# Performance work log

Hardware: AMD Instinct MI355X
Metric: run time of the kernel (lower is better)

The kernel has to match this reference:

```python
import jax, jax.numpy as jnp
import numpy as np

HID, NH, HD = 1024, 16, 64
WIN = 512
DFF, NE, TOPK = 4096, 8, 2
B, S = 1, 2048
EPS = 1e-6


def _rope_rotation_matrix(seq_len, head_dim):
    # Block-diagonal 2x2 rotation matrices per position (standard RoPE as a fused matrix).
    pos = np.arange(seq_len, dtype=np.float64)
    inv_freq = 1.0 / (10000.0 ** (np.arange(0, head_dim, 2, dtype=np.float64) / head_dim))
    ang = pos[:, None] * inv_freq[None, :]            # [S, HD/2]
    c, s = np.cos(ang), np.sin(ang)
    R = np.zeros((seq_len, head_dim, head_dim), np.float32)
    i = np.arange(0, head_dim, 2)
    R[:, i, i] = c
    R[:, i + 1, i + 1] = c
    R[:, i, i + 1] = -s
    R[:, i + 1, i] = s
    return jnp.asarray(R)


def setup_inputs() -> dict:
    key = jax.random.key(0)
    ks = jax.random.split(key, 10)
    init = lambda k, shape, scale=0.02: (jax.random.normal(k, shape, jnp.float32) * scale)
    return {
        "x": jax.random.normal(ks[0], (B, S, HID), jnp.float32),
        "rotation_matrix": _rope_rotation_matrix(S, HD),
        "rms1_w": jnp.ones((HID,), jnp.float32),
        "wq": init(ks[1], (HID, HID)),
        "wk": init(ks[2], (HID, HID)),
        "wv": init(ks[3], (HID, HID)),
        "wo": init(ks[4], (HID, HID)),
        "rms2_w": jnp.ones((HID,), jnp.float32),
        "gate_w": init(ks[5], (HID, NE)),
        "w1": init(ks[6], (NE, HID, DFF)),
        "w2": init(ks[7], (NE, DFF, HID)),
        "w3": init(ks[8], (NE, HID, DFF)),
    }


def _rmsnorm(x, w):
    return x * jax.lax.rsqrt(jnp.mean(x * x, axis=-1, keepdims=True) + EPS) * w


def reference(x, rotation_matrix, rms1_w, wq, wk, wv, wo, rms2_w, gate_w, w1, w2, w3):
    b, s, _ = x.shape
    # --- sliding-window attention with fused RoPE rotation matrix ---
    y = _rmsnorm(x, rms1_w)
    q = (y @ wq).reshape(b, s, NH, HD).transpose(0, 2, 1, 3)  # bhsd
    k = (y @ wk).reshape(b, s, NH, HD).transpose(0, 2, 1, 3)
    v = (y @ wv).reshape(b, s, NH, HD).transpose(0, 2, 1, 3)
    q = jnp.einsum('bhsd,sde->bhse', q, rotation_matrix)
    k = jnp.einsum('bhsd,sde->bhse', k, rotation_matrix)
    scores = jnp.einsum('bhqd,bhkd->bhqk', q, k) / np.float32(np.sqrt(HD))
    idx = jnp.arange(s)
    mask = (idx[:, None] >= idx[None, :]) & (idx[:, None] - idx[None, :] < WIN)
    scores = jnp.where(mask[None, None], scores, jnp.float32(-1e9))
    att = jax.nn.softmax(scores, axis=-1)
    attn_out = jnp.einsum('bhqk,bhkd->bhqd', att, v)
    attn_out = attn_out.transpose(0, 2, 1, 3).reshape(b, s, HID) @ wo
    x = x + attn_out
    # --- MoE SwiGLU FFN with top-k routing ---
    y = _rmsnorm(x, rms2_w)
    t = y.reshape(b * s, HID)                                  # [T, D]
    logits = t @ gate_w                                        # [T, E]
    top_v, top_i = jax.lax.top_k(logits, TOPK)
    gates = jax.nn.softmax(top_v, axis=-1)                     # [T, K]
    w_full = jnp.zeros((b * s, NE), t.dtype).at[
        jnp.arange(b * s)[:, None], top_i].set(gates)          # [T, E] sparse routing weights
    h = jax.nn.silu(jnp.einsum('td,edf->etf', t, w1)) * jnp.einsum('td,edf->etf', t, w3)
    expert_out = jnp.einsum('etf,efd->etd', h, w2)             # [E, T, D]
    moe = jnp.einsum('te,etd->td', w_full, expert_out).reshape(b, s, HID)
    return x + moe
```

## Files before the change

kernel.cpp:

```cpp
#include <hip/hip_runtime.h>
#include <hip/hip_bf16.h>
#include <stdint.h>


#define S_ 2048
#define HID_ 1024
#define NH_ 16
#define HD_ 64
#define WIN_ 512
#define DFF_ 4096
#define NE_ 8

typedef unsigned short u16;
typedef __attribute__((ext_vector_type(8))) short short8;
typedef __attribute__((ext_vector_type(4))) float f32x4;

__device__ __forceinline__ u16 f2bf(float f) {
  union { float f; unsigned u; } v; v.f = f;
  unsigned r = (v.u + 0x7FFFu + ((v.u >> 16) & 1u)) >> 16;
  return (u16)r;
}
__device__ __forceinline__ float bf2f(u16 b) {
  union { unsigned u; float f; } v; v.u = ((unsigned)b) << 16;
  return v.f;
}

__device__ __forceinline__ void gload16(const void* g, void* l) {
  __builtin_amdgcn_global_load_lds(
      (const __attribute__((address_space(1))) void*)g,
      (__attribute__((address_space(3))) void*)l, 16, 0, 0);
}

template <int N>
__device__ __forceinline__ void waitcnt_vm() {
  static_assert(N == 0 || N == 2 || N == 4 || N == 6 || N == 8 || N == 12 ||
                N == 16 || N == 24, "unsupported vmcnt");
  if constexpr (N == 0) asm volatile("s_waitcnt vmcnt(0)" ::: "memory");
  else if constexpr (N == 2) asm volatile("s_waitcnt vmcnt(2)" ::: "memory");
  else if constexpr (N == 4) asm volatile("s_waitcnt vmcnt(4)" ::: "memory");
  else if constexpr (N == 6) asm volatile("s_waitcnt vmcnt(6)" ::: "memory");
  else if constexpr (N == 8) asm volatile("s_waitcnt vmcnt(8)" ::: "memory");
  else if constexpr (N == 12) asm volatile("s_waitcnt vmcnt(12)" ::: "memory");
  else if constexpr (N == 16) asm volatile("s_waitcnt vmcnt(16)" ::: "memory");
  else if constexpr (N == 24) asm volatile("s_waitcnt vmcnt(24)" ::: "memory");
}

__global__ __launch_bounds__(512) void convT_f32_k(const float* __restrict__ Wa,
                                                   const float* __restrict__ Wb,
                                                   int zsplit,
                                                   u16* __restrict__ WT,
                                                   int K, int N, size_t matStride) {
  __shared__ alignas(16) char T[256 * 264];
  int z = blockIdx.z;
  const float* Wm = (z < zsplit ? Wa + (size_t)z * matStride
                                : Wb + (size_t)(z - zsplit) * matStride);
  u16* WTm = WT + (size_t)z * matStride;
  int n0 = blockIdx.x * 128, k0 = blockIdx.y * 256;
  int tid = threadIdx.x;
  int mq = tid & 31, tr_ = tid >> 5;
#pragma unroll
  for (int p = 0; p < 16; ++p) {
    int k = p * 16 + tr_;
    float4 v = *(const float4*)&Wm[(size_t)(k0 + k) * N + n0 + mq * 4];
    uint2 pk;
    pk.x = (unsigned)f2bf(v.x) | ((unsigned)f2bf(v.y) << 16);
    pk.y = (unsigned)f2bf(v.z) | ((unsigned)f2bf(v.w) << 16);
    *(uint2*)(T + k * 264 + ((mq ^ ((k >> 2) & 31)) << 3)) = pk;
  }
  __syncthreads();
#pragma unroll
  for (int p = 0; p < 8; ++p) {
    int n = p * 16 + tr_;
    int un = n >> 2, lo2 = (n & 3) * 2;
    short8 o;
#pragma unroll
    for (int j = 0; j < 8; ++j) {
      int k = mq * 8 + j;
      ((u16*)&o)[j] =
          *(const u16*)(T + k * 264 + ((un ^ ((k >> 2) & 31)) << 3) + lo2);
    }
    *(short8*)&WTm[(size_t)(n0 + n) * K + k0 + mq * 8] = o;
  }
}

__global__ __launch_bounds__(512) void convT_qkvo_k(const float* __restrict__ wq,
                                                    const float* __restrict__ wk,
                                                    const float* __restrict__ wv,
                                                    const float* __restrict__ wo,
                                                    u16* __restrict__ outT) {
  __shared__ alignas(16) char T[256 * 264];
  int z = blockIdx.z;
  const float* Wm = (z == 0) ? wq : (z == 1) ? wk : (z == 2) ? wv : wo;
  u16* WTm = outT + (size_t)z * HID_ * HID_;
  int n0 = blockIdx.x * 128, k0 = blockIdx.y * 256;
  int tid = threadIdx.x;
  int mq = tid & 31, tr_ = tid >> 5;
#pragma unroll
  for (int p = 0; p < 16; ++p) {
    int k = p * 16 + tr_;
    float4 v = *(const float4*)&Wm[(size_t)(k0 + k) * HID_ + n0 + mq * 4];
    uint2 pk;
    pk.x = (unsigned)f2bf(v.x) | ((unsigned)f2bf(v.y) << 16);
    pk.y = (unsigned)f2bf(v.z) | ((unsigned)f2bf(v.w) << 16);
    *(uint2*)(T + k * 264 + ((mq ^ ((k >> 2) & 31)) << 3)) = pk;
  }
  __syncthreads();
#pragma unroll
  for (int p = 0; p < 8; ++p) {
    int n = p * 16 + tr_;
    int un = n >> 2, lo2 = (n & 3) * 2;
    short8 o;
#pragma unroll
    for (int j = 0; j < 8; ++j) {
      int k = mq * 8 + j;
      ((u16*)&o)[j] =
          *(const u16*)(T + k * 264 + ((un ^ ((k >> 2) & 31)) << 3) + lo2);
    }
    *(short8*)&WTm[(size_t)(n0 + n) * HID_ + k0 + mq * 8] = o;
  }
}

__global__ __launch_bounds__(256) void convT_u16_k(const u16* __restrict__ W,
                                                   u16* __restrict__ WT,
                                                   int K, int N, size_t matStride) {
  __shared__ u16 t[64][66];
  const u16* Wm = W + (size_t)blockIdx.z * matStride;
  u16* WTm = WT + (size_t)blockIdx.z * matStride;
  int n0 = blockIdx.x * 64, k0 = blockIdx.y * 64;
  int tid = threadIdx.x;
  int c2 = (tid & 31) * 2, rr = tid >> 5;
#pragma unroll
  for (int it = 0; it < 8; ++it) {
    int r = it * 8 + rr;
    unsigned vv = *(const unsigned*)&Wm[(size_t)(k0 + r) * N + n0 + c2];
    t[c2][r] = (u16)vv;
    t[c2 + 1][r] = (u16)(vv >> 16);
  }
  __syncthreads();
#pragma unroll
  for (int it = 0; it < 8; ++it) {
    int n = it * 8 + rr;
    unsigned pk = (unsigned)t[n][c2] | ((unsigned)t[n][c2 + 1] << 16);
    *(unsigned*)&WTm[(size_t)(n0 + n) * K + k0 + c2] = pk;
  }
}

__global__ __launch_bounds__(256) void rope_tab_k(const float* __restrict__ rot,
                                                  float* __restrict__ cost,
                                                  float* __restrict__ sint) {
  int id = blockIdx.x * 256 + threadIdx.x;
  if (id >= S_ * 32) return;
  int s = id >> 5, j = id & 31;
  cost[id] = rot[(size_t)s * 4096 + (size_t)(2 * j) * 64 + 2 * j];
  sint[id] = rot[(size_t)s * 4096 + (size_t)(2 * j + 1) * 64 + 2 * j];
}

__global__ __launch_bounds__(256) void rms1_k(const float* __restrict__ x,
                                              const float* __restrict__ rw,
                                              u16* __restrict__ y) {
  int row = blockIdx.x, tid = threadIdx.x;
  const float4 v = *(const float4*)&x[(size_t)row * HID_ + tid * 4];
  float ss = v.x * v.x + v.y * v.y + v.z * v.z + v.w * v.w;
#pragma unroll
  for (int o = 32; o; o >>= 1) ss += __shfl_xor(ss, o);
  __shared__ float red[4];
  if ((tid & 63) == 0) red[tid >> 6] = ss;
  __syncthreads();
  float rstd = rsqrtf((red[0] + red[1] + red[2] + red[3]) * (1.f / HID_) + 1e-6f);
  const float4 w4 = *(const float4*)&rw[tid * 4];
  ushort4 o4;
  o4.x = f2bf(v.x * rstd * w4.x);
  o4.y = f2bf(v.y * rstd * w4.y);
  o4.z = f2bf(v.z * rstd * w4.z);
  o4.w = f2bf(v.w * rstd * w4.w);
  *(ushort4*)&y[(size_t)row * HID_ + tid * 4] = o4;
}

__global__ __launch_bounds__(256) void rms2_gate_k(const float* __restrict__ x2,
                                                   const float* __restrict__ rw,
                                                   const float* __restrict__ gw,
                                                   u16* __restrict__ y2,
                                                   float* __restrict__ logits) {
  int row = blockIdx.x, tid = threadIdx.x;
  int wv = tid >> 6, ln = tid & 63;
  const float4 v = *(const float4*)&x2[(size_t)row * HID_ + tid * 4];
  float ss = v.x * v.x + v.y * v.y + v.z * v.z + v.w * v.w;
#pragma unroll
  for (int o = 32; o; o >>= 1) ss += __shfl_xor(ss, o);
  __shared__ float red[4];
  __shared__ float lred[4][8];
  if (ln == 0) red[wv] = ss;
  __syncthreads();
  float rstd = rsqrtf((red[0] + red[1] + red[2] + red[3]) * (1.f / HID_) + 1e-6f);
  const float4 w4 = *(const float4*)&rw[tid * 4];
  float yv[4];
  yv[0] = v.x * rstd * w4.x; yv[1] = v.y * rstd * w4.y;
  yv[2] = v.z * rstd * w4.z; yv[3] = v.w * rstd * w4.w;
  ushort4 o4;
  o4.x = f2bf(yv[0]); o4.y = f2bf(yv[1]); o4.z = f2bf(yv[2]); o4.w = f2bf(yv[3]);
  *(ushort4*)&y2[(size_t)row * HID_ + tid * 4] = o4;
  float le[8] = {0, 0, 0, 0, 0, 0, 0, 0};
  int d0 = tid * 4;
#pragma unroll
  for (int j = 0; j < 4; ++j) {
    const float* grow = &gw[(size_t)(d0 + j) * NE_];
#pragma unroll
    for (int e = 0; e < 8; ++e) le[e] += yv[j] * grow[e];
  }
#pragma unroll
  for (int e = 0; e < 8; ++e) {
    float t = le[e];
#pragma unroll
    for (int o = 32; o; o >>= 1) t += __shfl_xor(t, o);
    le[e] = t;
  }
  if (ln == 0)
#pragma unroll
    for (int e = 0; e < 8; ++e) lred[wv][e] = le[e];
  __syncthreads();
  if (tid < 8)
    logits[(size_t)row * NE_ + tid] =
        lred[0][tid] + lred[1][tid] + lred[2][tid] + lred[3][tid];
}

__global__ __launch_bounds__(1024) void route_k(const float* __restrict__ logits,
                                                int* __restrict__ topi,
                                                float* __restrict__ topg,
                                                int* __restrict__ counts,
                                                int* __restrict__ ebase,
                                                int* __restrict__ slot_token,
                                                int* __restrict__ slot_of) {
  __shared__ int cnt[8], bas[8], rnk[8];
  int tid = threadIdx.x;
  if (tid < 8) { cnt[tid] = 0; rnk[tid] = 0; }
  __syncthreads();
  int e0[2], e1[2];
  float g0[2], g1[2];
#pragma unroll
  for (int s = 0; s < 2; ++s) {
    int t = tid * 2 + s;
    const float* lg = &logits[(size_t)t * NE_];
    float v0 = -1e30f; int i0 = 0;
#pragma unroll
    for (int e = 0; e < 8; ++e) {
      float x = lg[e];
      if (x > v0) { v0 = x; i0 = e; }
    }
    float v1 = -1e30f; int i1 = 0;
#pragma unroll
    for (int e = 0; e < 8; ++e) {
      if (e == i0) continue;
      float x = lg[e];
      if (x > v1) { v1 = x; i1 = e; }
    }
    float ex = __expf(v1 - v0);
    e0[s] = i0; e1[s] = i1;
    g0[s] = 1.f / (1.f + ex);
    g1[s] = ex / (1.f + ex);
    topi[t * 2] = i0; topi[t * 2 + 1] = i1;
    topg[t * 2] = g0[s]; topg[t * 2 + 1] = g1[s];
    atomicAdd(&cnt[i0], 1);
    atomicAdd(&cnt[i1], 1);
  }
  __syncthreads();
  if (tid == 0) {
    int s = 0;
    for (int e = 0; e < 8; ++e) { bas[e] = s; s += cnt[e]; }
  }
  __syncthreads();
#pragma unroll
  for (int s = 0; s < 2; ++s) {
    int t = tid * 2 + s;
    int p0 = bas[e0[s]] + atomicAdd(&rnk[e0[s]], 1);
    int p1 = bas[e1[s]] + atomicAdd(&rnk[e1[s]], 1);
    slot_token[p0] = t; slot_token[p1] = t;
    slot_of[t * 2] = p0; slot_of[t * 2 + 1] = p1;
  }
  if (tid < 8) { counts[tid] = cnt[tid]; ebase[tid] = bas[tid]; }
}

template <int MODE, int SLOTS>
__global__ __launch_bounds__(256, (SLOTS <= 3 ? 3 : (SLOTS <= 5 ? 2 : 1)))
void gemm3_k(
    const u16* __restrict__ A, const u16* __restrict__ B0,
    const u16* __restrict__ B1, const u16* __restrict__ B2, int K,
    const int* __restrict__ ecnt, const int* __restrict__ ebase,
    const float* __restrict__ cost, const float* __restrict__ sint,
    const float* __restrict__ xres, float* __restrict__ outf,
    u16* __restrict__ o0, u16* __restrict__ o1, u16* __restrict__ o2) {
  constexpr int WVM = 4 * (SLOTS - 2);
  __shared__ alignas(16) char smem[SLOTS * 16384];

  int n0 = blockIdx.x * 128, m0 = blockIdx.y * 128;
  int cnt = 0, base = 0, kc = 0;
  const u16* Bp;
  u16* outb = o0;
  float* pout = outf;
  int rope = 0;
  if constexpr (MODE == 0) {
    int z = blockIdx.z;
    Bp = (z == 0) ? B0 : (z == 1) ? B1 : B2;
    outb = (z == 0) ? o0 : (z == 1) ? o1 : o2;
    rope = (z < 2) ? 1 : 0;
  } else if constexpr (MODE == 1) {
    Bp = B0;
  } else if constexpr (MODE == 4) {
    int e = blockIdx.z >> 1;
    kc = blockIdx.z & 1;
    cnt = ecnt[e]; base = ebase[e];
    if (m0 >= cnt) return;
    Bp = B0 + (size_t)e * HID_ * DFF_;
    pout = outf + (size_t)kc * ((size_t)2 * S_ * HID_);
  } else {
    int e = blockIdx.z;
    cnt = ecnt[e]; base = ebase[e];
    if (m0 >= cnt) return;
    Bp = B0 + (size_t)e * HID_ * DFF_;
  }

  int tid = threadIdx.x, w = tid >> 6, l = tid & 63, lo = l & 15, g = l >> 4;
  int wm = w >> 1, wn = w & 1;
  int KT = K >> 5;
  size_t rb = (MODE == 4) ? (size_t)DFF_ * 2 : (size_t)K * 2;
  size_t kcoff = (MODE == 4) ? (size_t)kc * (size_t)(DFF_ / 2) * 2 : 0;

  int lrow = l >> 2, lu = l & 3;
  const char* pA[2];
  const char* pB[2];
  int ldOff[2];
#pragma unroll
  for (int j = 0; j < 2; ++j) {
    int rA = j * 64 + w * 16 + lrow;
    int swz = (lu ^ ((rA >> 1) & 3)) << 4;
    size_t arow;
    if constexpr (MODE == 3 || MODE == 4) {
      arow = (size_t)(base + min(m0 + rA, cnt - 1));
    } else {
      arow = (size_t)(m0 + rA);
    }
    pA[j] = (const char*)A + arow * rb + kcoff + swz;
    pB[j] = (const char*)Bp + (size_t)(n0 + rA) * rb + kcoff + swz;
    ldOff[j] = (j * 64 + w * 16) * 64;
  }

  auto stage = [&](int t) {
    char* s = smem + (t % SLOTS) * 16384;
    size_t kb = (size_t)t * 64;
    gload16(pA[0] + kb, s + ldOff[0]);
    gload16(pA[1] + kb, s + ldOff[1]);
    gload16(pB[0] + kb, s + 8192 + ldOff[0]);
    gload16(pB[1] + kb, s + 8192 + ldOff[1]);
  };

  f32x4 acc[4][4];
#pragma unroll
  for (int i = 0; i < 4; ++i)
#pragma unroll
    for (int j = 0; j < 4; ++j) acc[i][j] = (f32x4){0.f, 0.f, 0.f, 0.f};

#pragma unroll
  for (int s = 0; s < SLOTS - 1; ++s) stage(min(s, KT - 1));
  waitcnt_vm<WVM>();
  __builtin_amdgcn_s_barrier();

  for (int t = 0; t < KT; ++t) {
    char* s = smem + (t % SLOTS) * 16384;
    stage(min(t + SLOTS - 1, KT - 1));
    short8 afr[4], bfr[4];
#pragma unroll
    for (int mi = 0; mi < 4; ++mi) {
      int r = wm * 64 + mi * 16 + lo;
      afr[mi] = *(const short8*)(s + r * 64 + ((g ^ ((r >> 1) & 3)) << 4));
    }
#pragma unroll
    for (int ni = 0; ni < 4; ++ni) {
      int r = wn * 64 + ni * 16 + lo;
      bfr[ni] = *(const short8*)(s + 8192 + r * 64 + ((g ^ ((r >> 1) & 3)) << 4));
    }
    asm volatile("s_waitcnt lgkmcnt(0)" ::: "memory");
    __builtin_amdgcn_s_setprio(1);
#pragma unroll
    for (int mi = 0; mi < 4; ++mi)
#pragma unroll
      for (int ni = 0; ni < 4; ++ni)
        acc[mi][ni] = __builtin_amdgcn_mfma_f32_16x16x32_bf16(afr[mi], bfr[ni], acc[mi][ni], 0, 0, 0);
    __builtin_amdgcn_s_setprio(0);
    if (t + 1 < KT)
      waitcnt_vm<WVM>();
    else
      waitcnt_vm<0>();
    __builtin_amdgcn_s_barrier();
  }
  asm volatile("s_waitcnt vmcnt(0) lgkmcnt(0)" ::: "memory");

#pragma unroll
  for (int mi = 0; mi < 4; ++mi) {
    int lr = wm * 64 + mi * 16 + g * 4;
#pragma unroll
    for (int ni = 0; ni < 4; ++ni) {
      int c = n0 + wn * 64 + ni * 16 + lo;
#pragma unroll
      for (int r = 0; r < 4; ++r) {
        float v = acc[mi][ni][r];
        if constexpr (MODE == 0) {
          int row = m0 + lr + r;
          float p = __shfl_xor(v, 1);
          if (rope) {
            int dd = c & 63;
            float co = cost[(size_t)row * 32 + (dd >> 1)];
            float si = sint[(size_t)row * 32 + (dd >> 1)];
            v = (dd & 1) ? (co * v - si * p) : (co * v + si * p);
          }
          outb[((size_t)(c >> 6) * S_ + row) * HD_ + (c & 63)] = f2bf(v);
        } else if constexpr (MODE == 1) {
          int row = m0 + lr + r;
          outf[(size_t)row * HID_ + c] = v + xres[(size_t)row * HID_ + c];
        } else if constexpr (MODE == 4) {
          int m = m0 + lr + r;
          if (m < cnt) pout[(size_t)(base + m) * HID_ + c] = v;
        } else {
          int m = m0 + lr + r;
          if (m < cnt) outb[(size_t)(base + m) * HID_ + c] = f2bf(v);
        }
      }
    }
  }
}

__global__ __launch_bounds__(512, 2) void gemm5_k(
    const u16* __restrict__ A, const u16* __restrict__ B0,
    const u16* __restrict__ B1, int K, const int* __restrict__ ecnt,
    const int* __restrict__ ebase, const int* __restrict__ slot_token,
    u16* __restrict__ o0, u16* __restrict__ o1) {
  constexpr int BM = 256;
  constexpr int MROW = 128;
  constexpr int MI = 8;
  constexpr int MH = 4;
  constexpr int ABYTES = BM * 128;
  __shared__ alignas(16) char smem[ABYTES * 4];
  char* ldsA = smem;
  char* ldsB = smem + 2 * ABYTES;

  int n0 = blockIdx.x * BM, m0 = blockIdx.y * BM;
  int e = blockIdx.z >> 1, mat = blockIdx.z & 1;
  int cnt = ecnt[e], base = ebase[e];
  if (m0 >= cnt) return;
  const u16* Bp = (mat ? B1 : B0) + (size_t)e * DFF_ * HID_;
  u16* outb = mat ? o1 : o0;

  int tid = threadIdx.x, w = tid >> 6, l = tid & 63, lo = l & 15, g = l >> 4;
  int wm = w >> 2, wn = w & 3;
  int KT = K >> 6;
  size_t rb = (size_t)K * 2;

  int lrow = l >> 3, lu = l & 7;
  const char* pA[4];
  const char* pB[4];
  int ldOff[4];
#pragma unroll
  for (int j = 0; j < 4; ++j) {
    int rA = j * 64 + w * 8 + lrow;
    int swz = (lu ^ (rA & 7)) << 4;
    size_t arow = (size_t)slot_token[base + min(m0 + rA, cnt - 1)];
    pA[j] = (const char*)A + arow * rb + swz;
    pB[j] = (const char*)Bp + (size_t)(n0 + rA) * rb + swz;
    ldOff[j] = (j * 64 + w * 8) * 128;
  }

  auto stA = [&](int t, int j) {
    gload16(pA[j] + (size_t)t * 128, ldsA + (t & 1) * ABYTES + ldOff[j]);
  };
  auto stB = [&](int t, int j) {
    gload16(pB[j] + (size_t)t * 128, ldsB + (t & 1) * ABYTES + ldOff[j]);
  };
  auto rdA = [&](int d, int mi, int kh) {
    int row = wm * MROW + mi * 16 + lo;
    return *(const short8*)(ldsA + d * ABYTES + row * 128 +
                            (((kh * 4 + g) ^ (row & 7)) << 4));
  };
  auto rdB = [&](int d, int ni, int kh) {
    int row = wn * 64 + ni * 16 + lo;
    return *(const short8*)(ldsB + d * ABYTES + row * 128 +
                            (((kh * 4 + g) ^ (row & 7)) << 4));
  };

  f32x4 acc[MI][4];
#pragma unroll
  for (int i = 0; i < MI; ++i)
#pragma unroll
    for (int j = 0; j < 4; ++j) acc[i][j] = (f32x4){0.f, 0.f, 0.f, 0.f};

  stB(0, 0); stB(0, 1); stB(0, 2); stB(0, 3);
  stA(0, 0); stA(0, 2); stA(0, 1); stA(0, 3);
  waitcnt_vm<2>();
  __builtin_amdgcn_s_barrier();

  for (int t = 0; t < KT; ++t) {
    int d = t & 1;
    int tn = min(t + 1, KT - 1);
    short8 afr[MH][2], bfr[4][2];
    stB(tn, 0); stB(tn, 1); stB(tn, 2); stB(tn, 3);
#pragma unroll
    for (int i = 0; i < MH; ++i) {
      afr[i][0] = rdA(d, i, 0);
      afr[i][1] = rdA(d, i, 1);
    }
#pragma unroll
    for (int n = 0; n < 4; ++n) {
      bfr[n][0] = rdB(d, n, 0);
      bfr[n][1] = rdB(d, n, 1);
    }
    asm volatile("s_waitcnt lgkmcnt(0)" ::: "memory");
    __builtin_amdgcn_s_setprio(1);
#pragma unroll
    for (int kh = 0; kh < 2; ++kh)
#pragma unroll
      for (int i = 0; i < MH; ++i)
#pragma unroll
        for (int n = 0; n < 4; ++n)
          acc[i][n] = __builtin_amdgcn_mfma_f32_16x16x32_bf16(
              afr[i][kh], bfr[n][kh], acc[i][n], 0, 0, 0);
    __builtin_amdgcn_s_setprio(0);
    waitcnt_vm<4>();
    __builtin_amdgcn_s_barrier();
    stA(tn, 0); stA(tn, 2); stA(tn, 1); stA(tn, 3);
#pragma unroll
    for (int i = 0; i < MH; ++i) {
      afr[i][0] = rdA(d, MH + i, 0);
      afr[i][1] = rdA(d, MH + i, 1);
    }
    asm volatile("s_waitcnt lgkmcnt(0)" ::: "memory");
    __builtin_amdgcn_s_setprio(1);
#pragma unroll
    for (int kh = 0; kh < 2; ++kh)
#pragma unroll
      for (int i = 0; i < MH; ++i)
#pragma unroll
        for (int n = 0; n < 4; ++n)
          acc[MH + i][n] = __builtin_amdgcn_mfma_f32_16x16x32_bf16(
              afr[i][kh], bfr[n][kh], acc[MH + i][n], 0, 0, 0);
    __builtin_amdgcn_s_setprio(0);
    waitcnt_vm<2>();
    __builtin_amdgcn_s_barrier();
  }
  asm volatile("s_waitcnt vmcnt(0) lgkmcnt(0)" ::: "memory");

#pragma unroll
  for (int mi = 0; mi < MI; ++mi) {
    int lr = wm * MROW + mi * 16 + g * 4;
#pragma unroll
    for (int ni = 0; ni < 4; ++ni) {
      int c = n0 + wn * 64 + ni * 16 + lo;
#pragma unroll
      for (int r = 0; r < 4; ++r) {
        int m = m0 + lr + r;
        if (m < cnt) outb[(size_t)(base + m) * DFF_ + c] = f2bf(acc[mi][ni][r]);
      }
    }
  }
}

__global__ __launch_bounds__(256) void swiglu_k(u16* __restrict__ h1,
                                                const u16* __restrict__ h3) {
  size_t i = ((size_t)blockIdx.x * 256 + threadIdx.x) * 8;
  short8 a = *(const short8*)(h1 + i);
  short8 b = *(const short8*)(h3 + i);
  short8 o;
#pragma unroll
  for (int j = 0; j < 8; ++j) {
    float x = bf2f((u16)a[j]), y = bf2f((u16)b[j]);
    float s = x / (1.f + __expf(-x));
    o[j] = (short)f2bf(s * y);
  }
  *(short8*)(h1 + i) = o;
}

__global__ __launch_bounds__(256) void attn_k(const u16* __restrict__ qh,
                                              const u16* __restrict__ kh,
                                              const u16* __restrict__ vht,
                                              u16* __restrict__ attn) {
  int qt = blockIdx.x, h = blockIdx.y;
  int tid = threadIdx.x, w = tid >> 6, l = tid & 63, lo = l & 15, g = l >> 4;
  __shared__ alignas(16) char Ks[8192];
  __shared__ alignas(16) char Vs[8192];
  __shared__ alignas(16) char Ps[8192];
  char* Pw = Ps + w * 2048;
  int q0 = qt * 64, qw = q0 + w * 16;
  const u16* qhh = qh + ((size_t)h * S_ + qw) * HD_;
  short8 bq0 = *(const short8*)(qhh + lo * 64 + g * 8);
  short8 bq1 = *(const short8*)(qhh + lo * 64 + 32 + g * 8);
  int q = qw + lo;
  float m_run = -1e30f, l_run = 0.f;
  f32x4 o[4];
#pragma unroll
  for (int i = 0; i < 4; ++i) o[i] = (f32x4){0.f, 0.f, 0.f, 0.f};
  int kt0 = max(0, q0 - (WIN_ - 1)) >> 6;
  for (int kt = kt0; kt <= qt; ++kt) {
    int kb = kt * 64;
    {
      int r0 = w * 16 + (l >> 3), r1 = r0 + 8;
      int uu = l & 7;
      short8 k0v = *(const short8*)(kh + ((size_t)h * S_ + kb + r0) * HD_ + uu * 8);
      short8 k1v = *(const short8*)(kh + ((size_t)h * S_ + kb + r1) * HD_ + uu * 8);
      short8 v0v = *(const short8*)(vht + ((size_t)h * HD_ + r0) * S_ + kb + uu * 8);
      short8 v1v = *(const short8*)(vht + ((size_t)h * HD_ + r1) * S_ + kb + uu * 8);
      *(short8*)(Ks + r0 * 128 + ((uu ^ (r0 & 7)) << 4)) = k0v;
      *(short8*)(Ks + r1 * 128 + ((uu ^ (r1 & 7)) << 4)) = k1v;
      *(short8*)(Vs + r0 * 128 + ((uu ^ (r0 & 7)) << 4)) = v0v;
      *(short8*)(Vs + r1 * 128 + ((uu ^ (r1 & 7)) << 4)) = v1v;
    }
    __syncthreads();
    f32x4 st[4];
#pragma unroll
    for (int kf = 0; kf < 4; ++kf) {
      int key = kf * 16 + lo;
      short8 a0 = *(const short8*)(Ks + key * 128 + ((g ^ (key & 7)) << 4));
      short8 a1 = *(const short8*)(Ks + key * 128 + (((4 + g) ^ (key & 7)) << 4));
      f32x4 z = (f32x4){0.f, 0.f, 0.f, 0.f};
      z = __builtin_amdgcn_mfma_f32_16x16x32_bf16(a0, bq0, z, 0, 0, 0);
      z = __builtin_amdgcn_mfma_f32_16x16x32_bf16(a1, bq1, z, 0, 0, 0);
      st[kf] = z;
    }
    float p[16];
    float tmax = -1e30f;
#pragma unroll
    for (int kf = 0; kf < 4; ++kf)
#pragma unroll
      for (int r = 0; r < 4; ++r) {
        int key = kb + kf * 16 + g * 4 + r;
        float s = st[kf][r] * 0.125f;
        bool okm = (key <= q) && (q - key < WIN_);
        s = okm ? s : -1e30f;
        p[kf * 4 + r] = s;
        tmax = fmaxf(tmax, s);
      }
    tmax = fmaxf(tmax, __shfl_xor(tmax, 16));
    tmax = fmaxf(tmax, __shfl_xor(tmax, 32));
    float m_new = fmaxf(m_run, tmax);
    float corr = __expf(m_run - m_new);
    float tsum = 0.f;
#pragma unroll
    for (int i = 0; i < 16; ++i) {
      float pe = (p[i] > -1e29f) ? __expf(p[i] - m_new) : 0.f;
      p[i] = pe;
      tsum += pe;
    }
    tsum += __shfl_xor(tsum, 16);
    tsum += __shfl_xor(tsum, 32);
    l_run = l_run * corr + tsum;
    m_run = m_new;
#pragma unroll
    for (int kf = 0; kf < 4; ++kf)
#pragma unroll
      for (int pr = 0; pr < 2; ++pr) {
        int keyloc = kf * 16 + g * 4 + pr * 2;
        unsigned pk = (unsigned)f2bf(p[kf * 4 + pr * 2]) |
                      ((unsigned)f2bf(p[kf * 4 + pr * 2 + 1]) << 16);
        *(unsigned*)(Pw + lo * 128 + (((keyloc >> 3) ^ (lo & 7)) << 4) +
                     (keyloc & 7) * 2) = pk;
      }
    float c0 = __shfl(corr, g * 4 + 0), c1 = __shfl(corr, g * 4 + 1);
    float c2 = __shfl(corr, g * 4 + 2), c3 = __shfl(corr, g * 4 + 3);
#pragma unroll
    for (int nf = 0; nf < 4; ++nf) {
      o[nf][0] *= c0; o[nf][1] *= c1; o[nf][2] *= c2; o[nf][3] *= c3;
    }
    short8 ap0 = *(const short8*)(Pw + lo * 128 + ((g ^ (lo & 7)) << 4));
    short8 ap1 = *(const short8*)(Pw + lo * 128 + (((4 + g) ^ (lo & 7)) << 4));
#pragma unroll
    for (int nf = 0; nf < 4; ++nf) {
      int d = nf * 16 + lo;
      short8 v0 = *(const short8*)(Vs + d * 128 + ((g ^ (d & 7)) << 4));
      short8 v1 = *(const short8*)(Vs + d * 128 + (((4 + g) ^ (d & 7)) << 4));
      o[nf] = __builtin_amdgcn_mfma_f32_16x16x32_bf16(ap0, v0, o[nf], 0, 0, 0);
      o[nf] = __builtin_amdgcn_mfma_f32_16x16x32_bf16(ap1, v1, o[nf], 0, 0, 0);
    }
    __syncthreads();
  }
  float linv = 1.f / l_run;
  float i0 = __shfl(linv, g * 4 + 0), i1 = __shfl(linv, g * 4 + 1);
  float i2 = __shfl(linv, g * 4 + 2), i3 = __shfl(linv, g * 4 + 3);
#pragma unroll
  for (int nf = 0; nf < 4; ++nf) {
    int d = nf * 16 + lo;
    attn[(size_t)(qw + g * 4 + 0) * HID_ + h * HD_ + d] = f2bf(o[nf][0] * i0);
    attn[(size_t)(qw + g * 4 + 1) * HID_ + h * HD_ + d] = f2bf(o[nf][1] * i1);
    attn[(size_t)(qw + g * 4 + 2) * HID_ + h * HD_ + d] = f2bf(o[nf][2] * i2);
    attn[(size_t)(qw + g * 4 + 3) * HID_ + h * HD_ + d] = f2bf(o[nf][3] * i3);
  }
}

__global__ __launch_bounds__(256) void combine_k(float* __restrict__ out,
                                                 const float* __restrict__ part,
                                                 const int* __restrict__ slot_of,
                                                 const float* __restrict__ topg) {
  int row = blockIdx.x, tid = threadIdx.x;
  int d0 = tid * 4;
  const size_t PS = (size_t)2 * S_ * HID_;
  int p0 = slot_of[row * 2], p1 = slot_of[row * 2 + 1];
  float g0 = topg[row * 2], g1 = topg[row * 2 + 1];
  float4 cur = *(float4*)&out[(size_t)row * HID_ + d0];
  float4 a0 = *(const float4*)&part[(size_t)p0 * HID_ + d0];
  float4 a1 = *(const float4*)&part[PS + (size_t)p0 * HID_ + d0];
  float4 b0 = *(const float4*)&part[(size_t)p1 * HID_ + d0];
  float4 b1 = *(const float4*)&part[PS + (size_t)p1 * HID_ + d0];
  cur.x += g0 * (a0.x + a1.x) + g1 * (b0.x + b1.x);
  cur.y += g0 * (a0.y + a1.y) + g1 * (b0.y + b1.y);
  cur.z += g0 * (a0.z + a1.z) + g1 * (b0.z + b1.z);
  cur.w += g0 * (a0.w + a1.w) + g1 * (b0.w + b1.w);
  *(float4*)&out[(size_t)row * HID_ + d0] = cur;
}

extern "C" void kernel_launch(void* const* d_in, const int* in_sizes, int n_in,
                              void* d_out, int out_size, void* d_ws,
                              size_t ws_size, hipStream_t stream) {
  const float* x = (const float*)d_in[0];
  const float* rot = (const float*)d_in[1];
  const float* r1w = (const float*)d_in[2];
  const float* wq = (const float*)d_in[3];
  const float* wk = (const float*)d_in[4];
  const float* wv = (const float*)d_in[5];
  const float* wo = (const float*)d_in[6];
  const float* r2w = (const float*)d_in[7];
  const float* gw = (const float*)d_in[8];
  const float* w1 = (const float*)d_in[9];
  const float* w2 = (const float*)d_in[10];
  const float* w3 = (const float*)d_in[11];
  float* out = (float*)d_out;

  char* ws = (char*)d_ws;
  size_t off = 0;
  auto alloc = [&](size_t bytes) {
    char* p = ws + off;
    off += (bytes + 255) & ~(size_t)255;
    return p;
  };
  const size_t MB4 = (size_t)S_ * HID_ * 2;
  u16* wqkvoT = (u16*)alloc((size_t)4 * HID_ * HID_ * 2);
  u16* wqT = wqkvoT;
  u16* wkT = wqkvoT + (size_t)HID_ * HID_;
  u16* wvT = wqkvoT + (size_t)2 * HID_ * HID_;
  u16* woT = wqkvoT + (size_t)3 * HID_ * HID_;
  u16* w13T = (u16*)alloc((size_t)2 * NE_ * DFF_ * HID_ * 2);
  u16* w1T = w13T;
  u16* w3T = w13T + (size_t)NE_ * DFF_ * HID_;
  u16* w2T = (u16*)alloc((size_t)NE_ * HID_ * DFF_ * 2);
  char* uni = alloc((size_t)2 * S_ * DFF_ * 2);
  u16* ybf = (u16*)(uni);
  u16* qh = (u16*)(uni + MB4);
  u16* kh = (u16*)(uni + 2 * MB4);
  u16* vh = (u16*)(uni + 3 * MB4);
  u16* vht = (u16*)(uni + 4 * MB4);
  u16* attnb = (u16*)(uni + 5 * MB4);
  u16* h3 = (u16*)uni;
  float* partials = (float*)uni;
  u16* y2bf = (u16*)alloc(MB4);
  u16* h1 = (u16*)alloc((size_t)2 * S_ * DFF_ * 2);
  float* cost = (float*)alloc((size_t)S_ * 32 * 4);
  float* sint = (float*)alloc((size_t)S_ * 32 * 4);
  float* logits = (float*)alloc((size_t)S_ * NE_ * 4);
  int* topi = (int*)alloc((size_t)S_ * 2 * 4);
  float* topg = (float*)alloc((size_t)S_ * 2 * 4);
  int* ints = (int*)alloc(256);
  int* counts = ints;
  int* ebase = ints + 8;
  int* slot_token = (int*)alloc((size_t)2 * S_ * 4);
  int* slot_of = (int*)alloc((size_t)S_ * 2 * 4);
  (void)ws_size; (void)in_sizes; (void)n_in; (void)out_size;

  convT_qkvo_k<<<dim3(8, 4, 4), 512, 0, stream>>>(wq, wk, wv, wo, wqkvoT);
  convT_f32_k<<<dim3(32, 4, 16), 512, 0, stream>>>(w1, w3, 8, w13T, HID_, DFF_,
                                                   (size_t)HID_ * DFF_);
  convT_f32_k<<<dim3(8, 16, 8), 512, 0, stream>>>(w2, nullptr, 8, w2T, DFF_,
                                                  HID_, (size_t)DFF_ * HID_);

  rope_tab_k<<<dim3(256), 256, 0, stream>>>(rot, cost, sint);
  rms1_k<<<dim3(S_), 256, 0, stream>>>(x, r1w, ybf);

  gemm3_k<0, 5><<<dim3(8, 16, 3), 256, 0, stream>>>(
      ybf, wqT, wkT, wvT, HID_, nullptr, nullptr, cost, sint, nullptr,
      nullptr, qh, kh, vh);
  convT_u16_k<<<dim3(1, 32, 16), 256, 0, stream>>>(vh, vht, S_, HD_, (size_t)S_ * HD_);

  attn_k<<<dim3(32, 16), 256, 0, stream>>>(qh, kh, vht, attnb);

  gemm3_k<1, 5><<<dim3(8, 16, 1), 256, 0, stream>>>(
      attnb, woT, nullptr, nullptr, HID_, nullptr, nullptr, nullptr, nullptr,
      x, out, nullptr, nullptr, nullptr);

  rms2_gate_k<<<dim3(S_), 256, 0, stream>>>(out, r2w, gw, y2bf, logits);
  route_k<<<dim3(1), 1024, 0, stream>>>(logits, topi, topg, counts, ebase,
                                        slot_token, slot_of);

  gemm5_k<<<dim3(16, 8, 16), 512, 0, stream>>>(
      y2bf, w1T, w3T, HID_, counts, ebase, slot_token, h1, h3);
  swiglu_k<<<dim3(8192), 256, 0, stream>>>(h1, h3);
  gemm3_k<4, 4><<<dim3(8, 16, 16), 256, 0, stream>>>(
      h1, w2T, nullptr, nullptr, DFF_ / 2, counts, ebase, nullptr, nullptr,
      nullptr, partials, nullptr, nullptr, nullptr);
  combine_k<<<dim3(S_), 256, 0, stream>>>(out, partials, slot_of, topg);
}
```

Baseline: 422.1 us.

## Fuse fp32 w1/w3 transpose-convert into expert up-projection GEMM B-tile loads

Drops the separate convT kernel that turned w1/w3 to transposed bf16. The gemm5 kernel now reads the fp32 expert weights directly into registers, converts them to bf16 and writes them transposed into swizzled LDS. B loads are prefetched two tiles ahead and the per-iteration schedule is reworked. This saves one full write and re-read of 128MB of bf16 weights. In exchange, each M-block re-reads fp32 weights at twice the bytes and adds conversion and LDS-store ALU work inside the GEMM loop.

```diff
diff --git a/kernel.cpp b/kernel.cpp
--- a/kernel.cpp
+++ b/kernel.cpp
@@ -428,8 +428,8 @@
 }
 
 __global__ __launch_bounds__(512, 2) void gemm5_k(
-    const u16* __restrict__ A, const u16* __restrict__ B0,
-    const u16* __restrict__ B1, int K, const int* __restrict__ ecnt,
+    const u16* __restrict__ A, const float* __restrict__ W1,
+    const float* __restrict__ W3, int K, const int* __restrict__ ecnt,
     const int* __restrict__ ebase, const int* __restrict__ slot_token,
     u16* __restrict__ o0, u16* __restrict__ o1) {
   constexpr int BM = 256;
@@ -445,7 +445,7 @@
   int e = blockIdx.z >> 1, mat = blockIdx.z & 1;
   int cnt = ecnt[e], base = ebase[e];
   if (m0 >= cnt) return;
-  const u16* Bp = (mat ? B1 : B0) + (size_t)e * DFF_ * HID_;
+  const float* Wf = (mat ? W3 : W1) + (size_t)e * HID_ * DFF_;
   u16* outb = mat ? o1 : o0;
 
   int tid = threadIdx.x, w = tid >> 6, l = tid & 63, lo = l & 15, g = l >> 4;
@@ -455,24 +455,42 @@
 
   int lrow = l >> 3, lu = l & 7;
   const char* pA[4];
-  const char* pB[4];
-  int ldOff[4];
+  int ldOffA[4];
 #pragma unroll
   for (int j = 0; j < 4; ++j) {
     int rA = j * 64 + w * 8 + lrow;
     int swz = (lu ^ (rA & 7)) << 4;
     size_t arow = (size_t)slot_token[base + min(m0 + rA, cnt - 1)];
     pA[j] = (const char*)A + arow * rb + swz;
-    pB[j] = (const char*)Bp + (size_t)(n0 + rA) * rb + swz;
-    ldOff[j] = (j * 64 + w * 8) * 128;
-  }
-
-  auto stA = [&](int t, int j) {
-    gload16(pA[j] + (size_t)t * 128, ldsA + (t & 1) * ABYTES + ldOff[j]);
+    ldOffA[j] = (j * 64 + w * 8) * 128;
+  }
+  auto stA = [&](int t) {
+#pragma unroll
+    for (int j = 0; j < 4; ++j)
+      gload16(pA[j] + (size_t)t * 128, ldsA + (t & 1) * ABYTES + ldOffA[j]);
   };
-  auto stB = [&](int t, int j) {
-    gload16(pB[j] + (size_t)t * 128, ldsB + (t & 1) * ABYTES + ldOff[j]);
+
+  const float* pB0 = Wf + (size_t)(w * 8) * DFF_ + n0 + l * 4;
+  float4 vB[8];
+  auto rlB = [&](int t) {
+#pragma unroll
+    for (int j = 0; j < 8; ++j)
+      vB[j] = *(const float4*)(pB0 + ((size_t)t * 64 + j) * DFF_);
   };
+  auto dwB = [&](int t) {
+    char* dst = ldsB + (t & 1) * ABYTES;
+#pragma unroll
+    for (int c = 0; c < 4; ++c) {
+      int np = l * 4 + c;
+      short8 pk;
+#pragma unroll
+      for (int j = 0; j < 8; ++j)
+        ((u16*)&pk)[j] = f2bf(((const float*)&vB[j])[c]);
+      *(short8*)(dst + np * 128 +
+                 ((w ^ ((np & 7) ^ ((np >> 3) & 7))) << 4)) = pk;
+    }
+  };
+
   auto rdA = [&](int d, int mi, int kh) {
     int row = wm * MROW + mi * 16 + lo;
     return *(const short8*)(ldsA + d * ABYTES + row * 128 +
@@ -481,7 +499,8 @@
   auto rdB = [&](int d, int ni, int kh) {
     int row = wn * 64 + ni * 16 + lo;
     return *(const short8*)(ldsB + d * ABYTES + row * 128 +
-                            (((kh * 4 + g) ^ (row & 7)) << 4));
+                            (((kh * 4 + g) ^ ((row & 7) ^ ((row >> 3) & 7)))
+                             << 4));
   };
 
   f32x4 acc[MI][4];
@@ -490,25 +509,33 @@
 #pragma unroll
     for (int j = 0; j < 4; ++j) acc[i][j] = (f32x4){0.f, 0.f, 0.f, 0.f};
 
-  stB(0, 0); stB(0, 1); stB(0, 2); stB(0, 3);
-  stA(0, 0); stA(0, 2); stA(0, 1); stA(0, 3);
-  waitcnt_vm<2>();
+  rlB(0);
+  stA(0);
+  waitcnt_vm<4>();
+  dwB(0);
+  rlB(min(1, KT - 1));
+  waitcnt_vm<8>();
+  asm volatile("s_waitcnt lgkmcnt(0)" ::: "memory");
   __builtin_amdgcn_s_barrier();
 
   for (int t = 0; t < KT; ++t) {
     int d = t & 1;
     int tn = min(t + 1, KT - 1);
-    short8 afr[MH][2], bfr[4][2];
-    stB(tn, 0); stB(tn, 1); stB(tn, 2); stB(tn, 3);
+    int tn2 = min(t + 2, KT - 1);
+    stA(tn);
+    waitcnt_vm<4>();
+    dwB(tn);
+    rlB(tn2);
+    short8 bfr[4][2], afr[MH][2];
+#pragma unroll
+    for (int n = 0; n < 4; ++n) {
+      bfr[n][0] = rdB(d, n, 0);
+      bfr[n][1] = rdB(d, n, 1);
+    }
 #pragma unroll
     for (int i = 0; i < MH; ++i) {
       afr[i][0] = rdA(d, i, 0);
       afr[i][1] = rdA(d, i, 1);
-    }
-#pragma unroll
-    for (int n = 0; n < 4; ++n) {
-      bfr[n][0] = rdB(d, n, 0);
-      bfr[n][1] = rdB(d, n, 1);
     }
     asm volatile("s_waitcnt lgkmcnt(0)" ::: "memory");
     __builtin_amdgcn_s_setprio(1);
@@ -521,9 +548,6 @@
           acc[i][n] = __builtin_amdgcn_mfma_f32_16x16x32_bf16(
               afr[i][kh], bfr[n][kh], acc[i][n], 0, 0, 0);
     __builtin_amdgcn_s_setprio(0);
-    waitcnt_vm<4>();
-    __builtin_amdgcn_s_barrier();
-    stA(tn, 0); stA(tn, 2); stA(tn, 1); stA(tn, 3);
 #pragma unroll
     for (int i = 0; i < MH; ++i) {
       afr[i][0] = rdA(d, MH + i, 0);
@@ -540,7 +564,7 @@
           acc[MH + i][n] = __builtin_amdgcn_mfma_f32_16x16x32_bf16(
               afr[i][kh], bfr[n][kh], acc[MH + i][n], 0, 0, 0);
     __builtin_amdgcn_s_setprio(0);
-    waitcnt_vm<2>();
+    waitcnt_vm<8>();
     __builtin_amdgcn_s_barrier();
   }
   asm volatile("s_waitcnt vmcnt(0) lgkmcnt(0)" ::: "memory");
@@ -741,9 +765,6 @@
   u16* wkT = wqkvoT + (size_t)HID_ * HID_;
   u16* wvT = wqkvoT + (size_t)2 * HID_ * HID_;
   u16* woT = wqkvoT + (size_t)3 * HID_ * HID_;
-  u16* w13T = (u16*)alloc((size_t)2 * NE_ * DFF_ * HID_ * 2);
-  u16* w1T = w13T;
-  u16* w3T = w13T + (size_t)NE_ * DFF_ * HID_;
   u16* w2T = (u16*)alloc((size_t)NE_ * HID_ * DFF_ * 2);
   char* uni = alloc((size_t)2 * S_ * DFF_ * 2);
   u16* ybf = (u16*)(uni);
@@ -769,8 +790,6 @@
   (void)ws_size; (void)in_sizes; (void)n_in; (void)out_size;
 
   convT_qkvo_k<<<dim3(8, 4, 4), 512, 0, stream>>>(wq, wk, wv, wo, wqkvoT);
-  convT_f32_k<<<dim3(32, 4, 16), 512, 0, stream>>>(w1, w3, 8, w13T, HID_, DFF_,
-                                                   (size_t)HID_ * DFF_);
   convT_f32_k<<<dim3(8, 16, 8), 512, 0, stream>>>(w2, nullptr, 8, w2T, DFF_,
                                                   HID_, (size_t)DFF_ * HID_);
 
@@ -793,7 +812,7 @@
                                         slot_token, slot_of);
 
   gemm5_k<<<dim3(16, 8, 16), 512, 0, stream>>>(
-      y2bf, w1T, w3T, HID_, counts, ebase, slot_token, h1, h3);
+      y2bf, w1, w3, HID_, counts, ebase, slot_token, h1, h3);
   swiglu_k<<<dim3(8192), 256, 0, stream>>>(h1, h3);
   gemm3_k<4, 4><<<dim3(8, 16, 16), 256, 0, stream>>>(
       h1, w2T, nullptr, nullptr, DFF_ / 2, counts, ebase, nullptr, nullptr,
```

Result: slower. 431.6 us (+2.2%).
